# Kernel optimization log

Measured on AMD Instinct MI355X. Metric: run time of the kernel, lower is better.

The kernel has to match this reference:

```python
import jax, jax.numpy as jnp
import numpy as np

B, T, P, U = 2, 50, 5111, 64


def setup_inputs() -> dict:
    key = jax.random.key(0)
    ks = jax.random.split(key, 12)
    data_target = jax.random.randint(ks[0], (B, T), 0, P)
    data_cor = jax.random.randint(ks[1], (B, T), 0, 2)
    # X: bi-LSTM max-pooled problem encodings [P, 2U]
    X = jax.random.normal(ks[2], (P, 2 * U), dtype=jnp.float32) * 0.1
    # cos_X: cosine similarity of X with itself (as in call_encode)
    norm = jnp.sqrt(jnp.sum(X * X, axis=1))
    cos_X = (X @ X.T) / (norm[:, None] * norm[None, :])
    # causal lower-triangular aggregation mask [T, T]
    trimatrix = jnp.tril(jnp.ones((T, T), dtype=jnp.float32))
    # frozen embedding2 table [2, 4U]
    emb2 = jax.random.uniform(ks[3], (2, 4 * U), minval=-1.0, maxval=1.0, dtype=jnp.float32)
    # LSTM params (keras gate order i,f,c,o), input dim 4U
    s = 0.1549193338
    Wk = jax.random.uniform(ks[4], (4 * U, 4 * U), minval=-s, maxval=s, dtype=jnp.float32)
    Wr = jax.random.normal(ks[5], (U, 4 * U), dtype=jnp.float32) * 0.05  # orthogonal-ish stand-in
    bl = jnp.concatenate([jnp.zeros((U,)), jnp.ones((U,)), jnp.zeros((2 * U,))]).astype(jnp.float32)  # unit forget bias
    s1 = 0.1732050808
    W1 = jax.random.uniform(ks[6], (3 * U, 50), minval=-s1, maxval=s1, dtype=jnp.float32)
    b1 = jnp.zeros((50,), dtype=jnp.float32)
    s2 = 0.3429971703
    W2 = jax.random.uniform(ks[7], (50, 1), minval=-s2, maxval=s2, dtype=jnp.float32)
    b2 = jnp.zeros((1,), dtype=jnp.float32)
    return {"data_target": data_target, "data_cor": data_cor, "num_pro": P,
            "X": X, "cos_X": cos_X, "trimatrix": trimatrix, "emb2": emb2,
            "Wk": Wk, "Wr": Wr, "bl": bl, "W1": W1, "b1": b1, "W2": W2, "b2": b2}


def _lstm(x, Wk, Wr, bl):
    # x: [B, T, D] -> h: [B, T, U]; keras LSTM math, gate order i,f,g,o
    u = Wr.shape[0]
    xT = jnp.swapaxes(x, 0, 1)  # [T, B, D]
    h0 = jnp.zeros((x.shape[0], u), x.dtype)
    c0 = jnp.zeros((x.shape[0], u), x.dtype)

    def step(carry, xt):
        h, c = carry
        z = xt @ Wk + h @ Wr + bl
        i, f, g, o = jnp.split(z, 4, axis=-1)
        c = jax.nn.sigmoid(f) * c + jax.nn.sigmoid(i) * jnp.tanh(g)
        h = jax.nn.sigmoid(o) * jnp.tanh(c)
        return (h, c), h

    _, hs = jax.lax.scan(step, (h0, c0), xT)
    return jnp.swapaxes(hs, 0, 1)


def reference(data_target, data_cor, num_pro, X, cos_X, trimatrix, emb2, Wk, Wr, bl, W1, b1, W2, b2):
    # one_hot @ X == gather
    t_X = X[data_target]                             # [B,T,2U]
    t_X = jnp.concatenate([t_X, t_X], axis=-1)       # [B,T,4U]
    xt = t_X * emb2[data_cor]                        # [B,T,4U]
    ht = _lstm(xt, Wk, Wr, bl)                       # [B,T,U]
    # attention aggregation: a[b,t,p] = cos_X[target[b,t], p]
    a = cos_X[data_target]                           # [B,T,P]
    # ajhj[b,s,p,u] = sum_t trimatrix[t,s] * a[b,t,p] * ht[b,t,u]
    ajhj = jnp.einsum('btp,btu,ts->bspu', a, ht, trimatrix)  # [B,T,P,U]
    XX = jnp.broadcast_to(X[None, None], (ajhj.shape[0], ajhj.shape[1], num_pro, X.shape[1]))
    hatt = jnp.concatenate([ajhj, XX], axis=-1)      # [B,T,P,3U]
    r = jax.nn.relu(hatt @ W1 + b1)                  # [B,T,P,50]
    r = r @ W2 + b2                                  # [B,T,P,1]
    return r
```

## Files before the change

kernel.cpp:

```cpp
#include <hip/hip_runtime.h>
#include <math.h>

#define B_ 2
#define T_ 50
#define P_ 5111
#define U_ 64
#define SC_ 10
#define CH_ 5

typedef float v2f __attribute__((ext_vector_type(2)));

#define QPERM(x, ctrl)                                                        \
  __int_as_float(__builtin_amdgcn_mov_dpp(__float_as_int(x), (ctrl), 0xf, 0xf, true))

__global__ __launch_bounds__(256) void pre_kernel(
    const int* __restrict__ tgt, const int* __restrict__ cor,
    const float* __restrict__ X, const float* __restrict__ emb2,
    const float* __restrict__ Wk, float* __restrict__ ZX,
    const float* __restrict__ W1, const float* __restrict__ b1,
    float* __restrict__ XWT) {
  const int blk = blockIdx.x;
  const int k   = threadIdx.x;
  __shared__ float smem[512];

  if (blk < B_ * T_) {
    const int t_ = tgt[blk], c_ = cor[blk];
    smem[k] = X[t_ * 128 + (k & 127)] * emb2[c_ * 256 + k];
    __syncthreads();
    float z = 0.f;
#pragma unroll 8
    for (int d = 0; d < 256; ++d)
      z = fmaf(smem[d], Wk[d * 256 + k], z);
    ZX[blk * 256 + k] = z;
    return;
  }

  const int xb   = blk - B_ * T_;
  const int sub  = k >> 6, lane = k & 63;
  const int p    = xb * 4 + sub;
  float* xrow = &smem[sub * 128];
  if (p < P_) {
    xrow[lane]      = X[p * 128 + lane];
    xrow[64 + lane] = X[p * 128 + 64 + lane];
  }
  __syncthreads();
  if (p < P_ && lane < 50) {
    float acc = b1[lane];
#pragma unroll 16
    for (int u = 0; u < 128; ++u)
      acc = fmaf(xrow[u], W1[(64 + u) * 50 + lane], acc);
    XWT[lane * P_ + p] = acc;
  }
}

__global__ __launch_bounds__(256) void lstm_kernel(
    const float* __restrict__ ZX, const float* __restrict__ Wr,
    const float* __restrict__ bl, const float* __restrict__ W1,
    float* __restrict__ G) {
  const int b = blockIdx.x;
  const int k = threadIdx.x;
  const int g   = k & 3;
  const int u   = k >> 2;
  const int col = g * 64 + u;
  __shared__ __align__(16) float H_s[T_ + 1][64];
  __shared__ __align__(16) float W1_s[64 * 50];

  v2f w2[32];
#pragma unroll
  for (int i = 0; i < 32; ++i) {
    v2f t; t.x = Wr[(2 * i) * 256 + col]; t.y = Wr[(2 * i + 1) * 256 + col];
    w2[i] = t;
  }
  const float blv = bl[col];
  float znext = ZX[(b * T_) * 256 + col];
  for (int i = k; i < 64 * 50; i += 256) W1_s[i] = W1[i];
  if (k < 64) H_s[0][k] = 0.f;
  float c = 0.f;
  __syncthreads();

  for (int t = 0; t < T_; ++t) {
    const float zcur = znext;
    if (t + 1 < T_) znext = ZX[(b * T_ + t + 1) * 256 + col];
    const float4* h4 = (const float4*)&H_s[t][0];
    v2f a0 = {0.f, 0.f}, a1 = {0.f, 0.f}, a2 = {0.f, 0.f}, a3 = {0.f, 0.f};
#pragma unroll
    for (int q = 0; q < 16; ++q) {
      const float4 hq = h4[q];
      v2f hlo; hlo.x = hq.x; hlo.y = hq.y;
      v2f hhi; hhi.x = hq.z; hhi.y = hq.w;
      if (q & 1) {
        a2 = __builtin_elementwise_fma(hlo, w2[2 * q], a2);
        a3 = __builtin_elementwise_fma(hhi, w2[2 * q + 1], a3);
      } else {
        a0 = __builtin_elementwise_fma(hlo, w2[2 * q], a0);
        a1 = __builtin_elementwise_fma(hhi, w2[2 * q + 1], a1);
      }
    }
    const v2f as = (a0 + a2) + (a1 + a3);
    const float z = as.x + as.y + zcur + blv;
    const bool isg2 = (g == 2);
    const float arg = isg2 ? (2.f * z) : (-z);
    const float e   = __expf(arg);
    const float v   = __fdividef(1.f, 1.f + e);
    const float res = isg2 ? fmaf(-2.f, v, 1.f) : v;
    const float v1 = QPERM(res, 177);
    const float v2 = QPERM(res, 78);
    const float v3 = QPERM(res, 27);
    const float ig = (g == 0) ? res : (g == 1) ? v1 : (g == 2) ? v2 : v3;
    const float fg = (g == 1) ? res : (g == 0) ? v1 : (g == 3) ? v2 : v3;
    const float gg = (g == 2) ? res : (g == 3) ? v1 : (g == 0) ? v2 : v3;
    const float og = (g == 3) ? res : (g == 2) ? v1 : (g == 1) ? v2 : v3;
    c = fmaf(fg, c, ig * gg);
    const float th = fmaf(-2.f, __fdividef(1.f, 1.f + __expf(2.f * c)), 1.f);
    if (g == 0) H_s[t + 1][u] = og * th;
    __syncthreads();
  }

  const v2f* W1_2 = (const v2f*)W1_s;
  v2f*       G_2  = (v2f*)G;
  for (int task = k; task < T_ * 25; task += 256) {
    const int t  = task / 25;
    const int jp = task % 25;
    const float* hrow = &H_s[t + 1][0];
    v2f acc = {0.f, 0.f};
#pragma unroll
    for (int u2 = 0; u2 < 64; ++u2) {
      v2f hb; hb.x = hrow[u2]; hb.y = hrow[u2];
      acc = __builtin_elementwise_fma(hb, W1_2[u2 * 25 + jp], acc);
    }
    G_2[b * (T_ * 25) + task] = acc;
  }
}

template <int CH>
__device__ __forceinline__ void out_body(
    const int* __restrict__ tgt, const float* __restrict__ cosX,
    const float* __restrict__ G, const float* __restrict__ XWT,
    const float* __restrict__ W2, const float* __restrict__ b2,
    float* __restrict__ out, float* G_s, float* W2_s, int* tgt_s) {
  constexpr int s_lo = CH * SC_;
  constexpr int s_hi = s_lo + SC_;
  const int b   = blockIdx.y;
  const int tid = threadIdx.x;
  const int p   = blockIdx.x * 256 + tid;

  for (int i = s_lo * 50 + tid; i < T_ * 50; i += 256) G_s[i] = G[b * T_ * 50 + i];
  if (tid < 50) {
    W2_s[tid] = W2[tid];
    if (tid >= s_lo) tgt_s[tid] = tgt[b * T_ + tid];
  }
  __syncthreads();
  if (p >= P_) return;

  float av[T_ - s_lo];
#pragma unroll
  for (int t = s_lo; t < T_; ++t) av[t - s_lo] = cosX[tgt_s[t] * P_ + p];

  v2f S2[25];
#pragma unroll
  for (int jj = 0; jj < 25; ++jj) {
    v2f t; t.x = XWT[(2 * jj) * P_ + p]; t.y = XWT[(2 * jj + 1) * P_ + p];
    S2[jj] = t;
  }

#pragma unroll
  for (int t = T_ - 1; t >= s_hi; --t) {
    const v2f* G2 = (const v2f*)&G_s[t * 50];
    v2f av2; av2.x = av[t - s_lo]; av2.y = av[t - s_lo];
#pragma unroll
    for (int jj = 0; jj < 25; ++jj)
      S2[jj] = __builtin_elementwise_fma(av2, G2[jj], S2[jj]);
  }

  const v2f* W2_2 = (const v2f*)W2_s;
  const float b2v = b2[0];
  const v2f zero2 = {0.f, 0.f};
#pragma unroll
  for (int s = s_hi - 1; s >= s_lo; --s) {
    const v2f* G2 = (const v2f*)&G_s[s * 50];
    v2f av2; av2.x = av[s - s_lo]; av2.y = av[s - s_lo];
    v2f acc2; acc2.x = b2v; acc2.y = 0.f;
#pragma unroll
    for (int jj = 0; jj < 25; ++jj) {
      S2[jj] = __builtin_elementwise_fma(av2, G2[jj], S2[jj]);
      const v2f r = __builtin_elementwise_max(S2[jj], zero2);
      acc2 = __builtin_elementwise_fma(r, W2_2[jj], acc2);
    }
    out[(b * T_ + s) * P_ + p] = acc2.x + acc2.y;
  }
}

__global__ __launch_bounds__(256) void out_kernel(
    const int* __restrict__ tgt, const float* __restrict__ cosX,
    const float* __restrict__ G, const float* __restrict__ XWT,
    const float* __restrict__ W2, const float* __restrict__ b2,
    float* __restrict__ out) {
  __shared__ __align__(16) float G_s[T_ * 50];
  __shared__ __align__(16) float W2_s[50];
  __shared__ int tgt_s[T_];
  switch (blockIdx.z) {
    case 0: out_body<0>(tgt, cosX, G, XWT, W2, b2, out, G_s, W2_s, tgt_s); break;
    case 1: out_body<1>(tgt, cosX, G, XWT, W2, b2, out, G_s, W2_s, tgt_s); break;
    case 2: out_body<2>(tgt, cosX, G, XWT, W2, b2, out, G_s, W2_s, tgt_s); break;
    case 3: out_body<3>(tgt, cosX, G, XWT, W2, b2, out, G_s, W2_s, tgt_s); break;
    default: out_body<4>(tgt, cosX, G, XWT, W2, b2, out, G_s, W2_s, tgt_s); break;
  }
}

extern "C" void kernel_launch(void* const* d_in, const int* in_sizes, int n_in,
                              void* d_out, int out_size, void* d_ws, size_t ws_size,
                              hipStream_t stream) {
  const int*   tgt  = (const int*)d_in[0];
  const int*   cor  = (const int*)d_in[1];
  const float* X    = (const float*)d_in[3];
  const float* cosX = (const float*)d_in[4];
  const float* emb2 = (const float*)d_in[6];
  const float* Wk   = (const float*)d_in[7];
  const float* Wr   = (const float*)d_in[8];
  const float* bl   = (const float*)d_in[9];
  const float* W1   = (const float*)d_in[10];
  const float* b1   = (const float*)d_in[11];
  const float* W2   = (const float*)d_in[12];
  const float* b2   = (const float*)d_in[13];
  float* out = (float*)d_out;

  float* ws  = (float*)d_ws;
  float* ZX  = ws;
  float* G   = ws + 25600;
  float* XWT = ws + 30600;

  const int xw_blocks = (P_ + 3) / 4;
  pre_kernel<<<dim3(B_ * T_ + xw_blocks), dim3(256), 0, stream>>>(
      tgt, cor, X, emb2, Wk, ZX, W1, b1, XWT);
  lstm_kernel<<<dim3(B_), dim3(256), 0, stream>>>(ZX, Wr, bl, W1, G);
  out_kernel<<<dim3((P_ + 255) / 256, B_, CH_), dim3(256), 0, stream>>>(
      tgt, cosX, G, XWT, W2, b2, out);
}
```

Baseline: 226.8 us.

## Overlap X·W1 projection with serial LSTM recurrence in one launch

Moves the per-problem X·W1 projection out of the pre-kernel and into the LSTM launch, where 254 extra blocks grid-stride over the problems while two blocks run the serial 50-step recurrence. The aim is to hide the latency-bound LSTM behind useful parallel work and shorten the first kernel to just the input projection. It also raises wave priority during the recurrence and defers the W1 shared-memory load until after the loop. The risk is that the co-resident projection blocks contend for the CUs running the LSTM and slow its critical path.

```diff
diff --git a/kernel.cpp b/kernel.cpp
--- a/kernel.cpp
+++ b/kernel.cpp
@@ -13,57 +13,60 @@
 #define QPERM(x, ctrl)                                                        \
   __int_as_float(__builtin_amdgcn_mov_dpp(__float_as_int(x), (ctrl), 0xf, 0xf, true))
 
-__global__ __launch_bounds__(256) void pre_kernel(
+__global__ __launch_bounds__(256) void zx_kernel(
     const int* __restrict__ tgt, const int* __restrict__ cor,
     const float* __restrict__ X, const float* __restrict__ emb2,
-    const float* __restrict__ Wk, float* __restrict__ ZX,
-    const float* __restrict__ W1, const float* __restrict__ b1,
-    float* __restrict__ XWT) {
+    const float* __restrict__ Wk, float* __restrict__ ZX) {
+  const int bt = blockIdx.x;
+  const int k  = threadIdx.x;
+  __shared__ float xe[256];
+  const int t_ = tgt[bt], c_ = cor[bt];
+  xe[k] = X[t_ * 128 + (k & 127)] * emb2[c_ * 256 + k];
+  __syncthreads();
+  float z = 0.f;
+#pragma unroll 8
+  for (int d = 0; d < 256; ++d)
+    z = fmaf(xe[d], Wk[d * 256 + k], z);
+  ZX[bt * 256 + k] = z;
+}
+
+__global__ __launch_bounds__(256) void lstm_xwt_kernel(
+    const float* __restrict__ ZX, const float* __restrict__ Wr,
+    const float* __restrict__ bl, const float* __restrict__ W1,
+    const float* __restrict__ X, const float* __restrict__ b1,
+    float* __restrict__ G, float* __restrict__ XWT) {
   const int blk = blockIdx.x;
   const int k   = threadIdx.x;
-  __shared__ float smem[512];
-
-  if (blk < B_ * T_) {
-    const int t_ = tgt[blk], c_ = cor[blk];
-    smem[k] = X[t_ * 128 + (k & 127)] * emb2[c_ * 256 + k];
-    __syncthreads();
-    float z = 0.f;
-#pragma unroll 8
-    for (int d = 0; d < 256; ++d)
-      z = fmaf(smem[d], Wk[d * 256 + k], z);
-    ZX[blk * 256 + k] = z;
+  __shared__ __align__(16) float H_s[T_ + 1][64];
+  __shared__ __align__(16) float W1_s[64 * 50];
+  __shared__ float xrow_s[4][128];
+
+  if (blk >= B_) {
+    const int sub = k >> 6, lane = k & 63;
+    const int nq  = (P_ + 3) / 4;
+    for (int q = blk - B_; q < nq; q += 254) {
+      const int p = q * 4 + sub;
+      if (p < P_) {
+        xrow_s[sub][lane]      = X[p * 128 + lane];
+        xrow_s[sub][64 + lane] = X[p * 128 + 64 + lane];
+      }
+      __syncthreads();
+      if (p < P_ && lane < 50) {
+        float acc = b1[lane];
+#pragma unroll 16
+        for (int u = 0; u < 128; ++u)
+          acc = fmaf(xrow_s[sub][u], W1[(64 + u) * 50 + lane], acc);
+        XWT[lane * P_ + p] = acc;
+      }
+      __syncthreads();
+    }
     return;
   }
 
-  const int xb   = blk - B_ * T_;
-  const int sub  = k >> 6, lane = k & 63;
-  const int p    = xb * 4 + sub;
-  float* xrow = &smem[sub * 128];
-  if (p < P_) {
-    xrow[lane]      = X[p * 128 + lane];
-    xrow[64 + lane] = X[p * 128 + 64 + lane];
-  }
-  __syncthreads();
-  if (p < P_ && lane < 50) {
-    float acc = b1[lane];
-#pragma unroll 16
-    for (int u = 0; u < 128; ++u)
-      acc = fmaf(xrow[u], W1[(64 + u) * 50 + lane], acc);
-    XWT[lane * P_ + p] = acc;
-  }
-}
-
-__global__ __launch_bounds__(256) void lstm_kernel(
-    const float* __restrict__ ZX, const float* __restrict__ Wr,
-    const float* __restrict__ bl, const float* __restrict__ W1,
-    float* __restrict__ G) {
-  const int b = blockIdx.x;
-  const int k = threadIdx.x;
+  const int b   = blk;
   const int g   = k & 3;
   const int u   = k >> 2;
   const int col = g * 64 + u;
-  __shared__ __align__(16) float H_s[T_ + 1][64];
-  __shared__ __align__(16) float W1_s[64 * 50];
 
   v2f w2[32];
 #pragma unroll
@@ -73,11 +76,11 @@
   }
   const float blv = bl[col];
   float znext = ZX[(b * T_) * 256 + col];
-  for (int i = k; i < 64 * 50; i += 256) W1_s[i] = W1[i];
   if (k < 64) H_s[0][k] = 0.f;
   float c = 0.f;
   __syncthreads();
 
+  __builtin_amdgcn_s_setprio(1);
   for (int t = 0; t < T_; ++t) {
     const float zcur = znext;
     if (t + 1 < T_) znext = ZX[(b * T_ + t + 1) * 256 + col];
@@ -115,6 +118,10 @@
     if (g == 0) H_s[t + 1][u] = og * th;
     __syncthreads();
   }
+  __builtin_amdgcn_s_setprio(0);
+
+  for (int i = k; i < 64 * 50; i += 256) W1_s[i] = W1[i];
+  __syncthreads();
 
   const v2f* W1_2 = (const v2f*)W1_s;
   v2f*       G_2  = (v2f*)G;
@@ -229,10 +236,9 @@
   float* G   = ws + 25600;
   float* XWT = ws + 30600;
 
-  const int xw_blocks = (P_ + 3) / 4;
-  pre_kernel<<<dim3(B_ * T_ + xw_blocks), dim3(256), 0, stream>>>(
-      tgt, cor, X, emb2, Wk, ZX, W1, b1, XWT);
-  lstm_kernel<<<dim3(B_), dim3(256), 0, stream>>>(ZX, Wr, bl, W1, G);
+  zx_kernel<<<dim3(B_ * T_), dim3(256), 0, stream>>>(tgt, cor, X, emb2, Wk, ZX);
+  lstm_xwt_kernel<<<dim3(256), dim3(256), 0, stream>>>(
+      ZX, Wr, bl, W1, X, b1, G, XWT);
   out_kernel<<<dim3((P_ + 255) / 256, B_, CH_), dim3(256), 0, stream>>>(
       tgt, cosX, G, XWT, W2, b2, out);
 }
```

After: 227.4 us. About the same (+0.2%).
